# Kernel tuning notes

Measured on AMD Instinct MI355X. Metric: run time of the kernel, lower is better.

Reference implementation:

```python
import jax, jax.numpy as jnp
import numpy as np
import math

B, S, E, DH = 4, 2048, 2048, 256
NEG_INF = jnp.float32(-jnp.inf)


def setup_inputs() -> dict:
    key = jax.random.key(0)
    kx, kq, kk, kv, kp = jax.random.split(key, 5)
    xav = math.sqrt(6.0 / (E + DH))  # xavier_uniform bound
    x = jax.random.normal(kx, (B, S, E), dtype=jnp.float32)
    W_Q = jax.random.uniform(kq, (E, DH), dtype=jnp.float32, minval=-xav, maxval=xav)
    W_K = jax.random.uniform(kk, (E, DH), dtype=jnp.float32, minval=-xav, maxval=xav)
    W_V = jax.random.uniform(kv, (E, DH), dtype=jnp.float32, minval=-xav, maxval=xav)
    b_Q = jnp.zeros((DH,), dtype=jnp.float32)
    b_K = jnp.zeros((DH,), dtype=jnp.float32)
    b_V = jnp.zeros((DH,), dtype=jnp.float32)
    causal_mask = jnp.tril(jnp.ones((S, S), dtype=jnp.int32))  # 1 = attend
    padding_mask = jax.random.randint(kp, (B, S), 0, 2) == 1  # True = masked key
    padding_mask = padding_mask.at[:, 0].set(False)  # keep key 0 valid (avoid all--inf rows)
    return {"x": x, "causal_mask": causal_mask, "padding_mask": padding_mask,
            "W_Q": W_Q, "b_Q": b_Q, "W_K": W_K, "b_K": b_K, "W_V": W_V, "b_V": b_V}


def reference(x, causal_mask, padding_mask, W_Q, b_Q, W_K, b_K, W_V, b_V):
    # Q, K, V projections: [B,S,E] @ [E,DH] -> [B,S,DH]
    Q = x @ W_Q + b_Q
    K = x @ W_K + b_K
    V = x @ W_V + b_V
    scores = jnp.einsum('bqd,bkd->bqk', Q, K) / jnp.sqrt(jnp.float32(DH))
    scores = jnp.where(causal_mask[None, :, :] == 0, NEG_INF, scores)
    scores = jnp.where(padding_mask[:, None, :], NEG_INF, scores)
    attn = jax.nn.softmax(scores, axis=-1)
    return attn @ V  # [B,S,DH]
```

## Files before the change

kernel.cpp:

```cpp
#include <hip/hip_runtime.h>
#include <stdint.h>

typedef float  f32x4  __attribute__((ext_vector_type(4)));
typedef short  s16x8  __attribute__((ext_vector_type(8)));
typedef unsigned int u32x4 __attribute__((ext_vector_type(4)));
typedef unsigned short ushort_t;

#define B_  4
#define S_  2048
#define E_  2048
#define DH_ 256

#define MFMA16(a,b,c) __builtin_amdgcn_mfma_f32_16x16x32_bf16((a),(b),(c),0,0,0)

__device__ __forceinline__ ushort_t f2b(float f){
  unsigned u = __builtin_bit_cast(unsigned, f);
  u += 0x7fffu + ((u >> 16) & 1u);
  return (ushort_t)(u >> 16);
}

__global__ __launch_bounds__(256) void k_convert_x(const float* __restrict__ x,
                                                   ushort_t* __restrict__ xbf){
  size_t i = ((size_t)blockIdx.x * 256 + threadIdx.x) * 8;
  f32x4 a = *(const f32x4*)(x + i);
  f32x4 b = *(const f32x4*)(x + i + 4);
  union { ushort_t us[8]; u32x4 v; } u;
#pragma unroll
  for (int j = 0; j < 4; ++j){ u.us[j] = f2b(a[j]); u.us[4+j] = f2b(b[j]); }
  *(u32x4*)(xbf + i) = u.v;
}

__global__ __launch_bounds__(256) void k_transpose_w(const float* __restrict__ Wq,
                                                     const float* __restrict__ Wk,
                                                     const float* __restrict__ Wv,
                                                     ushort_t* __restrict__ Wt){
  __shared__ ushort_t tile[32][33];
  int z = blockIdx.z;
  const float* W = (z == 0) ? Wq : ((z == 1) ? Wk : Wv);
  int k0 = blockIdx.x * 32, n0 = blockIdx.y * 32;
  int t = threadIdx.x, tx = t & 31, ty = t >> 5;
#pragma unroll
  for (int i = 0; i < 4; ++i)
    tile[ty + i*8][tx] = f2b(W[(size_t)(k0 + ty + i*8) * DH_ + n0 + tx]);
  __syncthreads();
#pragma unroll
  for (int i = 0; i < 4; ++i)
    Wt[(size_t)z * DH_ * E_ + (size_t)(n0 + ty + i*8) * E_ + k0 + tx] = tile[tx][ty + i*8];
}

__global__ __launch_bounds__(256) void k_prep_pad(const unsigned char* __restrict__ pm,
                                                  float* __restrict__ padf){
  const int n = B_ * S_;
  int any = 0;
  for (int i = threadIdx.x; i < n; i += 256)
    if ((i & 3) && pm[i]) any = 1;
  int isb = __syncthreads_or(any);
  for (int i = threadIdx.x; i < n; i += 256){
    unsigned char v = isb ? pm[i] : pm[(size_t)i * 4];
    padf[i] = v ? -__builtin_inff() : 0.0f;
  }
}

__global__ __launch_bounds__(256) void k_gemm_qkv(const ushort_t* __restrict__ xbf,
                                                  const ushort_t* __restrict__ Wt,
                                                  const float* __restrict__ bQ,
                                                  const float* __restrict__ bK,
                                                  const float* __restrict__ bV,
                                                  ushort_t* __restrict__ Qo,
                                                  ushort_t* __restrict__ Ko,
                                                  ushort_t* __restrict__ Vo){
  __shared__ __align__(16) ushort_t Al[64 * 64];
  __shared__ __align__(16) ushort_t Bl[64 * 64];
  int z = blockIdx.z;
  const ushort_t* W = Wt + (size_t)z * DH_ * E_;
  const float* bias = (z == 0) ? bQ : ((z == 1) ? bK : bV);
  ushort_t* out = (z == 0) ? Qo : ((z == 1) ? Ko : Vo);
  int m0 = blockIdx.x * 64, n0 = blockIdx.y * 64;
  int t = threadIdx.x;
  int lane = t & 63, w = t >> 6, lo = lane & 15, grp = lane >> 4;
  f32x4 z4; z4[0] = z4[1] = z4[2] = z4[3] = 0.f;
  f32x4 acc[4] = { z4, z4, z4, z4 };
  int arow = t >> 2;
  int c8a  = t & 3;

  for (int k0 = 0; k0 < E_; k0 += 64){
    __syncthreads();
#pragma unroll
    for (int p = 0; p < 2; ++p){
      int c8 = c8a + p * 4;
      u32x4 av = *(const u32x4*)(xbf + (size_t)(m0 + arow) * E_ + k0 + c8 * 8);
      *(u32x4*)((char*)Al + ((arow * 128 + c8 * 16) ^ ((arow & 7) << 4))) = av;
      u32x4 bv = *(const u32x4*)(W + (size_t)(n0 + arow) * E_ + k0 + c8 * 8);
      *(u32x4*)((char*)Bl + ((arow * 128 + c8 * 16) ^ ((arow & 7) << 4))) = bv;
    }
    __syncthreads();
#pragma unroll
    for (int kk = 0; kk < 2; ++kk){
      int ar = w * 16 + lo;
      s16x8 a = *(const s16x8*)((const char*)Al +
                 ((ar * 128 + kk * 64 + grp * 16) ^ ((ar & 7) << 4)));
#pragma unroll
      for (int nt = 0; nt < 4; ++nt){
        int br = nt * 16 + lo;
        s16x8 b = *(const s16x8*)((const char*)Bl +
                   ((br * 128 + kk * 64 + grp * 16) ^ ((br & 7) << 4)));
        acc[nt] = MFMA16(a, b, acc[nt]);
      }
    }
  }
#pragma unroll
  for (int nt = 0; nt < 4; ++nt){
    int col = n0 + nt * 16 + lo;
    float bb = bias[col];
#pragma unroll
    for (int r = 0; r < 4; ++r){
      int row = m0 + w * 16 + grp * 4 + r;
      out[(size_t)row * DH_ + col] = f2b(acc[nt][r] + bb);
    }
  }
}

__global__ __launch_bounds__(256) void k_transpose_v(const ushort_t* __restrict__ V,
                                                     ushort_t* __restrict__ Vt){
  __shared__ ushort_t tile[32][33];
  int r0 = blockIdx.x * 32, c0 = blockIdx.y * 32;
  int t = threadIdx.x, tx = t & 31, ty = t >> 5;
#pragma unroll
  for (int i = 0; i < 4; ++i)
    tile[ty + i*8][tx] = V[(size_t)(r0 + ty + i*8) * DH_ + c0 + tx];
  __syncthreads();
  int b = r0 >> 11, s0 = r0 & (S_ - 1);
#pragma unroll
  for (int i = 0; i < 4; ++i)
    Vt[(size_t)(b * DH_ + c0 + ty + i*8) * S_ + s0 + tx] = tile[tx][ty + i*8];
}

__global__ __launch_bounds__(512) void k_attn(const ushort_t* __restrict__ Q,
                                              const ushort_t* __restrict__ K,
                                              const ushort_t* __restrict__ Vt,
                                              const float* __restrict__ padf,
                                              float* __restrict__ out){
  __shared__ __align__(16) ushort_t P[8][16][32];
  __shared__ float Osum[16][260];
  __shared__ float ml[8][16][2];
  __shared__ float Linv[16];
  int blk = blockIdx.x;
  int b = blk & (B_ - 1);
  int qt = (S_ / 16 - 1) - (blk >> 2);
  int t = threadIdx.x;
  int lane = t & 63, w = t >> 6, lo = lane & 15, grp = lane >> 4;
  int qbase = qt * 16;
  const float NEG = -__builtin_inff();

  s16x8 aq[8];
#pragma unroll
  for (int d = 0; d < 8; ++d)
    aq[d] = *(const s16x8*)(Q + (size_t)(b * S_ + qbase + lo) * DH_ + d * 32 + grp * 8);

  f32x4 z4; z4[0] = z4[1] = z4[2] = z4[3] = 0.f;
  f32x4 o[16];
#pragma unroll
  for (int i = 0; i < 16; ++i) o[i] = z4;
  float m[4], l[4];
#pragma unroll
  for (int r = 0; r < 4; ++r){ m[r] = NEG; l[r] = 0.f; }

  int qhi = qbase + 15;
  int ntiles = (qhi >> 5) + 1;

  for (int kt = w; kt < ntiles; kt += 8){
    int k0 = kt * 32;
    f32x4 s[2];
#pragma unroll
    for (int h = 0; h < 2; ++h){
      int kb = k0 + h * 16;
      if (kb <= qhi){
        f32x4 acc = z4;
#pragma unroll
        for (int d = 0; d < 8; ++d){
          s16x8 bk = *(const s16x8*)(K + (size_t)(b * S_ + kb + lo) * DH_ + d * 32 + grp * 8);
          acc = MFMA16(aq[d], bk, acc);
        }
        int kcol = kb + lo;
        float pv = padf[b * S_ + kcol];
#pragma unroll
        for (int r = 0; r < 4; ++r){
          int q = qbase + grp * 4 + r;
          float v = acc[r] * 0.0625f + pv;
          s[h][r] = (kcol <= q) ? v : NEG;
        }
      } else {
#pragma unroll
        for (int r = 0; r < 4; ++r) s[h][r] = NEG;
      }
    }
    float alpha[4];
    int need = 0;
#pragma unroll
    for (int r = 0; r < 4; ++r){
      float mr = fmaxf(s[0][r], s[1][r]);
      mr = fmaxf(mr, __shfl_xor(mr, 1));
      mr = fmaxf(mr, __shfl_xor(mr, 2));
      mr = fmaxf(mr, __shfl_xor(mr, 4));
      mr = fmaxf(mr, __shfl_xor(mr, 8));
      float mn = fmaxf(m[r], mr);
      float mexp = (mn == NEG) ? 0.f : mn;
      float al = __expf(m[r] - mexp);
      alpha[r] = al;
      float p0 = __expf(s[0][r] - mexp);
      float p1 = __expf(s[1][r] - mexp);
      s[0][r] = p0; s[1][r] = p1;
      float pr = p0 + p1;
      pr += __shfl_xor(pr, 1);
      pr += __shfl_xor(pr, 2);
      pr += __shfl_xor(pr, 4);
      pr += __shfl_xor(pr, 8);
      l[r] = l[r] * al + pr;
      need |= (mn > m[r]);
      m[r] = mn;
    }
    if (__any(need)){
#pragma unroll
      for (int i = 0; i < 16; ++i)
#pragma unroll
        for (int r = 0; r < 4; ++r) o[i][r] *= alpha[r];
    }
#pragma unroll
    for (int h = 0; h < 2; ++h)
#pragma unroll
      for (int r = 0; r < 4; ++r)
        P[w][grp * 4 + r][h * 16 + lo] = f2b(s[h][r]);
    s16x8 pa = *(const s16x8*)(&P[w][lo][grp * 8]);
#pragma unroll
    for (int i = 0; i < 16; ++i){
      s16x8 vb = *(const s16x8*)(Vt + (size_t)(b * DH_ + i * 16 + lo) * S_ + k0 + grp * 8);
      o[i] = MFMA16(pa, vb, o[i]);
    }
  }

  if (lo == 0){
#pragma unroll
    for (int r = 0; r < 4; ++r){ ml[w][grp * 4 + r][0] = m[r]; ml[w][grp * 4 + r][1] = l[r]; }
  }
  __syncthreads();
  float sc[4];
#pragma unroll
  for (int r = 0; r < 4; ++r){
    int row = grp * 4 + r;
    float Mx = NEG;
#pragma unroll
    for (int ww = 0; ww < 8; ++ww) Mx = fmaxf(Mx, ml[ww][row][0]);
    float Ls = 0.f;
#pragma unroll
    for (int ww = 0; ww < 8; ++ww) Ls += ml[ww][row][1] * __expf(ml[ww][row][0] - Mx);
    sc[r] = __expf(m[r] - Mx);
    if (w == 0 && lo == 0) Linv[row] = 1.0f / Ls;
  }
#pragma unroll
  for (int i = 0; i < 16; ++i)
#pragma unroll
    for (int r = 0; r < 4; ++r) o[i][r] *= sc[r];
  for (int ww = 0; ww < 8; ++ww){
    if (w == ww){
#pragma unroll
      for (int i = 0; i < 16; ++i)
#pragma unroll
        for (int r = 0; r < 4; ++r){
          float* p = &Osum[grp * 4 + r][i * 16 + lo];
          if (ww == 0) *p = o[i][r]; else *p += o[i][r];
        }
    }
    __syncthreads();
  }
  int row = t >> 5, sub = t & 31;
  float li = Linv[row];
  size_t obase = (size_t)(b * S_ + qbase + row) * DH_ + sub * 8;
#pragma unroll
  for (int j = 0; j < 8; ++j)
    out[obase + j] = Osum[row][sub * 8 + j] * li;
}

extern "C" void kernel_launch(void* const* d_in, const int* in_sizes, int n_in,
                              void* d_out, int out_size, void* d_ws, size_t ws_size,
                              hipStream_t stream){
  const float* x          = (const float*)d_in[0];
  const unsigned char* pm = (const unsigned char*)d_in[2];
  const float* Wq = (const float*)d_in[3];
  const float* bQ = (const float*)d_in[4];
  const float* Wk = (const float*)d_in[5];
  const float* bK = (const float*)d_in[6];
  const float* Wv = (const float*)d_in[7];
  const float* bV = (const float*)d_in[8];
  float* out = (float*)d_out;

  char* ws = (char*)d_ws;
  ushort_t* xbf  = (ushort_t*)(ws);
  ushort_t* Wt   = (ushort_t*)(ws + 33554432);
  ushort_t* Qb   = (ushort_t*)(ws + 36700160);
  ushort_t* Kb   = (ushort_t*)(ws + 40894464);
  ushort_t* Vb   = (ushort_t*)(ws + 45088768);
  ushort_t* Vt   = (ushort_t*)(ws + 49283072);
  float*    padf = (float*)  (ws + 53477376);

  k_convert_x  <<<dim3(8192),       dim3(256), 0, stream>>>(x, xbf);
  k_transpose_w<<<dim3(64, 8, 3),   dim3(256), 0, stream>>>(Wq, Wk, Wv, Wt);
  k_prep_pad   <<<dim3(1),          dim3(256), 0, stream>>>(pm, padf);
  k_gemm_qkv   <<<dim3(128, 4, 3),  dim3(256), 0, stream>>>(xbf, Wt, bQ, bK, bV, Qb, Kb, Vb);
  k_transpose_v<<<dim3(256, 8),     dim3(256), 0, stream>>>(Vb, Vt);
  k_attn       <<<dim3(512),        dim3(512), 0, stream>>>(Qb, Kb, Vt, padf, out);
}
```

Before: 300.4 us.

## Enlarge GEMM tile with direct LDS loads and rework attention to 64-key tiles

The QKV GEMM now uses 128x64 tiles with a 2x2 wave layout and loads into LDS with global_load_lds, so the register round trip is dropped and each B tile is reused across more rows. Attention now processes 64-key tiles per wave and computes S transposed, so each lane owns one query row. It adds a lazy max-rescale rule with a threshold of 8 and applies the causal mask only on diagonal tiles. The padding mask is packed into bitmasks instead of a float array. The risks are more register pressure, and possible precision drift from the lazy rescale and the -1e30 sentinel.

```diff
diff --git a/kernel.cpp b/kernel.cpp
--- a/kernel.cpp
+++ b/kernel.cpp
@@ -5,6 +5,7 @@
 typedef short  s16x8  __attribute__((ext_vector_type(8)));
 typedef unsigned int u32x4 __attribute__((ext_vector_type(4)));
 typedef unsigned short ushort_t;
+typedef unsigned int uint_t;
 
 #define B_  4
 #define S_  2048
@@ -12,6 +13,10 @@
 #define DH_ 256
 
 #define MFMA16(a,b,c) __builtin_amdgcn_mfma_f32_16x16x32_bf16((a),(b),(c),0,0,0)
+
+#define GL16(gp, lp) __builtin_amdgcn_global_load_lds( \
+    (const __attribute__((address_space(1))) unsigned int*)(gp), \
+    (__attribute__((address_space(3))) unsigned int*)(lp), 16, 0, 0)
 
 __device__ __forceinline__ ushort_t f2b(float f){
   unsigned u = __builtin_bit_cast(unsigned, f);
@@ -49,16 +54,22 @@
 }
 
 __global__ __launch_bounds__(256) void k_prep_pad(const unsigned char* __restrict__ pm,
-                                                  float* __restrict__ padf){
+                                                  uint_t* __restrict__ padbits){
   const int n = B_ * S_;
   int any = 0;
   for (int i = threadIdx.x; i < n; i += 256)
     if ((i & 3) && pm[i]) any = 1;
   int isb = __syncthreads_or(any);
-  for (int i = threadIdx.x; i < n; i += 256){
-    unsigned char v = isb ? pm[i] : pm[(size_t)i * 4];
-    padf[i] = v ? -__builtin_inff() : 0.0f;
-  }
+  int t = threadIdx.x;
+  uint_t bits = 0;
+  int base = (t >> 6) * S_ + (t & 63) * 32;
+#pragma unroll
+  for (int j = 0; j < 32; ++j){
+    size_t idx = base + j;
+    unsigned char v = isb ? pm[idx] : pm[idx * 4];
+    bits |= (v ? 1u : 0u) << j;
+  }
+  padbits[t] = bits;
 }
 
 __global__ __launch_bounds__(256) void k_gemm_qkv(const ushort_t* __restrict__ xbf,
@@ -69,54 +80,69 @@
                                                   ushort_t* __restrict__ Qo,
                                                   ushort_t* __restrict__ Ko,
                                                   ushort_t* __restrict__ Vo){
-  __shared__ __align__(16) ushort_t Al[64 * 64];
+  __shared__ __align__(16) ushort_t Al[128 * 64];
   __shared__ __align__(16) ushort_t Bl[64 * 64];
   int z = blockIdx.z;
   const ushort_t* W = Wt + (size_t)z * DH_ * E_;
   const float* bias = (z == 0) ? bQ : ((z == 1) ? bK : bV);
   ushort_t* out = (z == 0) ? Qo : ((z == 1) ? Ko : Vo);
-  int m0 = blockIdx.x * 64, n0 = blockIdx.y * 64;
+  int m0 = blockIdx.x * 128, n0 = blockIdx.y * 64;
   int t = threadIdx.x;
   int lane = t & 63, w = t >> 6, lo = lane & 15, grp = lane >> 4;
+  int wm = w >> 1, wn = w & 1;
+  int rA = t >> 3;
+  int jsw = ((t & 7) ^ (rA & 7)) * 8;
+
   f32x4 z4; z4[0] = z4[1] = z4[2] = z4[3] = 0.f;
-  f32x4 acc[4] = { z4, z4, z4, z4 };
-  int arow = t >> 2;
-  int c8a  = t & 3;
+  f32x4 acc[4][2];
+#pragma unroll
+  for (int mt = 0; mt < 4; ++mt){ acc[mt][0] = z4; acc[mt][1] = z4; }
+
+  char* lA = (char*)Al + w * 1024;
+  char* lB = (char*)Bl + w * 1024;
 
   for (int k0 = 0; k0 < E_; k0 += 64){
     __syncthreads();
-#pragma unroll
-    for (int p = 0; p < 2; ++p){
-      int c8 = c8a + p * 4;
-      u32x4 av = *(const u32x4*)(xbf + (size_t)(m0 + arow) * E_ + k0 + c8 * 8);
-      *(u32x4*)((char*)Al + ((arow * 128 + c8 * 16) ^ ((arow & 7) << 4))) = av;
-      u32x4 bv = *(const u32x4*)(W + (size_t)(n0 + arow) * E_ + k0 + c8 * 8);
-      *(u32x4*)((char*)Bl + ((arow * 128 + c8 * 16) ^ ((arow & 7) << 4))) = bv;
-    }
+    const ushort_t* gA = xbf + (size_t)(m0 + rA) * E_ + k0 + jsw;
+    const ushort_t* gB = W   + (size_t)(n0 + rA) * E_ + k0 + jsw;
+#pragma unroll
+    for (int i = 0; i < 4; ++i)
+      GL16(gA + (size_t)i * 32 * E_, lA + i * 4096);
+#pragma unroll
+    for (int i = 0; i < 2; ++i)
+      GL16(gB + (size_t)i * 32 * E_, lB + i * 4096);
     __syncthreads();
 #pragma unroll
     for (int kk = 0; kk < 2; ++kk){
-      int ar = w * 16 + lo;
-      s16x8 a = *(const s16x8*)((const char*)Al +
-                 ((ar * 128 + kk * 64 + grp * 16) ^ ((ar & 7) << 4)));
-#pragma unroll
-      for (int nt = 0; nt < 4; ++nt){
-        int br = nt * 16 + lo;
-        s16x8 b = *(const s16x8*)((const char*)Bl +
-                   ((br * 128 + kk * 64 + grp * 16) ^ ((br & 7) << 4)));
-        acc[nt] = MFMA16(a, b, acc[nt]);
-      }
-    }
-  }
-#pragma unroll
-  for (int nt = 0; nt < 4; ++nt){
-    int col = n0 + nt * 16 + lo;
+      s16x8 av[4], bv[2];
+#pragma unroll
+      for (int mt = 0; mt < 4; ++mt){
+        int row = wm * 64 + mt * 16 + lo;
+        av[mt] = *(const s16x8*)((char*)Al + ((row * 128 + kk * 64 + grp * 16) ^ ((row & 7) << 4)));
+      }
+#pragma unroll
+      for (int nt = 0; nt < 2; ++nt){
+        int row = wn * 32 + nt * 16 + lo;
+        bv[nt] = *(const s16x8*)((char*)Bl + ((row * 128 + kk * 64 + grp * 16) ^ ((row & 7) << 4)));
+      }
+#pragma unroll
+      for (int mt = 0; mt < 4; ++mt)
+#pragma unroll
+        for (int nt = 0; nt < 2; ++nt)
+          acc[mt][nt] = MFMA16(av[mt], bv[nt], acc[mt][nt]);
+    }
+  }
+#pragma unroll
+  for (int nt = 0; nt < 2; ++nt){
+    int col = n0 + wn * 32 + nt * 16 + lo;
     float bb = bias[col];
 #pragma unroll
-    for (int r = 0; r < 4; ++r){
-      int row = m0 + w * 16 + grp * 4 + r;
-      out[(size_t)row * DH_ + col] = f2b(acc[nt][r] + bb);
-    }
+    for (int mt = 0; mt < 4; ++mt)
+#pragma unroll
+      for (int r = 0; r < 4; ++r){
+        int row = m0 + wm * 64 + mt * 16 + grp * 4 + r;
+        out[(size_t)row * DH_ + col] = f2b(acc[mt][nt][r] + bb);
+      }
   }
 }
 
@@ -138,9 +164,9 @@
 __global__ __launch_bounds__(512) void k_attn(const ushort_t* __restrict__ Q,
                                               const ushort_t* __restrict__ K,
                                               const ushort_t* __restrict__ Vt,
-                                              const float* __restrict__ padf,
+                                              const uint_t* __restrict__ padbits,
                                               float* __restrict__ out){
-  __shared__ __align__(16) ushort_t P[8][16][32];
+  __shared__ __align__(16) ushort_t P[8][16][72];
   __shared__ float Osum[16][260];
   __shared__ float ml[8][16][2];
   __shared__ float Linv[16];
@@ -151,6 +177,7 @@
   int lane = t & 63, w = t >> 6, lo = lane & 15, grp = lane >> 4;
   int qbase = qt * 16;
   const float NEG = -__builtin_inff();
+  const float MSENT = -1e30f;
 
   s16x8 aq[8];
 #pragma unroll
@@ -161,105 +188,124 @@
   f32x4 o[16];
 #pragma unroll
   for (int i = 0; i < 16; ++i) o[i] = z4;
-  float m[4], l[4];
-#pragma unroll
-  for (int r = 0; r < 4; ++r){ m[r] = NEG; l[r] = 0.f; }
+  float m_lo = MSENT, l_lo = 0.f;
 
   int qhi = qbase + 15;
-  int ntiles = (qhi >> 5) + 1;
-
-  for (int kt = w; kt < ntiles; kt += 8){
-    int k0 = kt * 32;
-    f32x4 s[2];
-#pragma unroll
-    for (int h = 0; h < 2; ++h){
-      int kb = k0 + h * 16;
-      if (kb <= qhi){
-        f32x4 acc = z4;
-#pragma unroll
-        for (int d = 0; d < 8; ++d){
-          s16x8 bk = *(const s16x8*)(K + (size_t)(b * S_ + kb + lo) * DH_ + d * 32 + grp * 8);
-          acc = MFMA16(aq[d], bk, acc);
-        }
-        int kcol = kb + lo;
-        float pv = padf[b * S_ + kcol];
-#pragma unroll
-        for (int r = 0; r < 4; ++r){
-          int q = qbase + grp * 4 + r;
-          float v = acc[r] * 0.0625f + pv;
-          s[h][r] = (kcol <= q) ? v : NEG;
-        }
-      } else {
-#pragma unroll
-        for (int r = 0; r < 4; ++r) s[h][r] = NEG;
-      }
-    }
-    float alpha[4];
-    int need = 0;
-#pragma unroll
-    for (int r = 0; r < 4; ++r){
-      float mr = fmaxf(s[0][r], s[1][r]);
-      mr = fmaxf(mr, __shfl_xor(mr, 1));
-      mr = fmaxf(mr, __shfl_xor(mr, 2));
-      mr = fmaxf(mr, __shfl_xor(mr, 4));
-      mr = fmaxf(mr, __shfl_xor(mr, 8));
-      float mn = fmaxf(m[r], mr);
-      float mexp = (mn == NEG) ? 0.f : mn;
-      float al = __expf(m[r] - mexp);
-      alpha[r] = al;
-      float p0 = __expf(s[0][r] - mexp);
-      float p1 = __expf(s[1][r] - mexp);
-      s[0][r] = p0; s[1][r] = p1;
-      float pr = p0 + p1;
-      pr += __shfl_xor(pr, 1);
-      pr += __shfl_xor(pr, 2);
-      pr += __shfl_xor(pr, 4);
-      pr += __shfl_xor(pr, 8);
-      l[r] = l[r] * al + pr;
-      need |= (mn > m[r]);
-      m[r] = mn;
-    }
-    if (__any(need)){
-#pragma unroll
-      for (int i = 0; i < 16; ++i)
-#pragma unroll
-        for (int r = 0; r < 4; ++r) o[i][r] *= alpha[r];
-    }
-#pragma unroll
-    for (int h = 0; h < 2; ++h)
-#pragma unroll
-      for (int r = 0; r < 4; ++r)
-        P[w][grp * 4 + r][h * 16 + lo] = f2b(s[h][r]);
-    s16x8 pa = *(const s16x8*)(&P[w][lo][grp * 8]);
+  int nt64 = (qhi >> 6) + 1;
+
+  for (int kt = w; kt < nt64; kt += 8){
+    int k0 = kt * 64;
+    bool full = (k0 + 63 <= qbase);
+    f32x4 sc[4];
+#pragma unroll
+    for (int h = 0; h < 4; ++h) sc[h] = z4;
+#pragma unroll
+    for (int d = 0; d < 8; ++d){
+#pragma unroll
+      for (int h = 0; h < 4; ++h){
+        s16x8 kf = *(const s16x8*)(K + (size_t)(b * S_ + k0 + h * 16 + lo) * DH_ + d * 32 + grp * 8);
+        sc[h] = MFMA16(kf, aq[d], sc[h]);
+      }
+    }
+    uint_t pb0 = padbits[b * 64 + kt * 2];
+    uint_t pb1 = padbits[b * 64 + kt * 2 + 1];
+#pragma unroll
+    for (int h = 0; h < 4; ++h){
+      uint_t bg = ((h < 2 ? pb0 : pb1) >> ((h & 1) * 16)) >> (4 * grp);
+#pragma unroll
+      for (int r = 0; r < 4; ++r){
+        float v = sc[h][r] * 0.0625f;
+        sc[h][r] = ((bg >> r) & 1) ? NEG : v;
+      }
+    }
+    if (!full){
+#pragma unroll
+      for (int h = 0; h < 4; ++h)
+#pragma unroll
+        for (int r = 0; r < 4; ++r)
+          if (k0 + h * 16 + 4 * grp + r > qbase + lo) sc[h][r] = NEG;
+    }
+    float mt0 = fmaxf(fmaxf(sc[0][0], sc[0][1]), fmaxf(sc[0][2], sc[0][3]));
+    float mt1 = fmaxf(fmaxf(sc[1][0], sc[1][1]), fmaxf(sc[1][2], sc[1][3]));
+    float mt2 = fmaxf(fmaxf(sc[2][0], sc[2][1]), fmaxf(sc[2][2], sc[2][3]));
+    float mt3 = fmaxf(fmaxf(sc[3][0], sc[3][1]), fmaxf(sc[3][2], sc[3][3]));
+    float mt = fmaxf(fmaxf(mt0, mt1), fmaxf(mt2, mt3));
+    mt = fmaxf(mt, __shfl_xor(mt, 16));
+    mt = fmaxf(mt, __shfl_xor(mt, 32));
+    if (__any(mt > m_lo + 8.f)){
+      float mn = fmaxf(m_lo, mt);
+      float al = __expf(m_lo - mn);
+      m_lo = mn;
+      l_lo *= al;
+      float a0 = __shfl(al, 4 * grp + 0);
+      float a1 = __shfl(al, 4 * grp + 1);
+      float a2 = __shfl(al, 4 * grp + 2);
+      float a3 = __shfl(al, 4 * grp + 3);
+#pragma unroll
+      for (int i = 0; i < 16; ++i){
+        o[i][0] *= a0; o[i][1] *= a1; o[i][2] *= a2; o[i][3] *= a3;
+      }
+    }
+    float ls = 0.f;
+#pragma unroll
+    for (int h = 0; h < 4; ++h)
+#pragma unroll
+      for (int r = 0; r < 4; ++r){
+        float p = __expf(sc[h][r] - m_lo);
+        sc[h][r] = p;
+        ls += p;
+      }
+    ls += __shfl_xor(ls, 16);
+    ls += __shfl_xor(ls, 32);
+    l_lo += ls;
+    char* prow = (char*)&P[w][lo][0];
+#pragma unroll
+    for (int h = 0; h < 4; ++h){
+      uint_t u0 = (uint_t)f2b(sc[h][0]) | ((uint_t)f2b(sc[h][1]) << 16);
+      uint_t u1 = (uint_t)f2b(sc[h][2]) | ((uint_t)f2b(sc[h][3]) << 16);
+      *(uint_t*)(prow + h * 32 + grp * 8)     = u0;
+      *(uint_t*)(prow + h * 32 + grp * 8 + 4) = u1;
+    }
+    s16x8 pa0 = *(const s16x8*)(prow + grp * 16);
+    s16x8 pa1 = *(const s16x8*)(prow + 64 + grp * 16);
 #pragma unroll
     for (int i = 0; i < 16; ++i){
-      s16x8 vb = *(const s16x8*)(Vt + (size_t)(b * DH_ + i * 16 + lo) * S_ + k0 + grp * 8);
-      o[i] = MFMA16(pa, vb, o[i]);
-    }
+      s16x8 v0 = *(const s16x8*)(Vt + (size_t)(b * DH_ + i * 16 + lo) * S_ + k0 + grp * 8);
+      s16x8 v1 = *(const s16x8*)(Vt + (size_t)(b * DH_ + i * 16 + lo) * S_ + k0 + 32 + grp * 8);
+      o[i] = MFMA16(pa0, v0, o[i]);
+      o[i] = MFMA16(pa1, v1, o[i]);
+    }
+  }
+
+  float mo[4], lo_[4];
+#pragma unroll
+  for (int r = 0; r < 4; ++r){
+    mo[r]  = __shfl(m_lo, 4 * grp + r);
+    lo_[r] = __shfl(l_lo, 4 * grp + r);
   }
 
   if (lo == 0){
 #pragma unroll
-    for (int r = 0; r < 4; ++r){ ml[w][grp * 4 + r][0] = m[r]; ml[w][grp * 4 + r][1] = l[r]; }
+    for (int r = 0; r < 4; ++r){ ml[w][grp * 4 + r][0] = mo[r]; ml[w][grp * 4 + r][1] = lo_[r]; }
   }
   __syncthreads();
-  float sc[4];
+  float sc2[4];
 #pragma unroll
   for (int r = 0; r < 4; ++r){
     int row = grp * 4 + r;
-    float Mx = NEG;
+    float Mx = MSENT;
 #pragma unroll
     for (int ww = 0; ww < 8; ++ww) Mx = fmaxf(Mx, ml[ww][row][0]);
     float Ls = 0.f;
 #pragma unroll
     for (int ww = 0; ww < 8; ++ww) Ls += ml[ww][row][1] * __expf(ml[ww][row][0] - Mx);
-    sc[r] = __expf(m[r] - Mx);
+    sc2[r] = __expf(mo[r] - Mx);
     if (w == 0 && lo == 0) Linv[row] = 1.0f / Ls;
   }
 #pragma unroll
   for (int i = 0; i < 16; ++i)
 #pragma unroll
-    for (int r = 0; r < 4; ++r) o[i][r] *= sc[r];
+    for (int r = 0; r < 4; ++r) o[i][r] *= sc2[r];
   for (int ww = 0; ww < 8; ++ww){
     if (w == ww){
 #pragma unroll
@@ -300,12 +346,12 @@
   ushort_t* Kb   = (ushort_t*)(ws + 40894464);
   ushort_t* Vb   = (ushort_t*)(ws + 45088768);
   ushort_t* Vt   = (ushort_t*)(ws + 49283072);
-  float*    padf = (float*)  (ws + 53477376);
+  uint_t*   padbits = (uint_t*)(ws + 53477376);
 
   k_convert_x  <<<dim3(8192),       dim3(256), 0, stream>>>(x, xbf);
   k_transpose_w<<<dim3(64, 8, 3),   dim3(256), 0, stream>>>(Wq, Wk, Wv, Wt);
-  k_prep_pad   <<<dim3(1),          dim3(256), 0, stream>>>(pm, padf);
-  k_gemm_qkv   <<<dim3(128, 4, 3),  dim3(256), 0, stream>>>(xbf, Wt, bQ, bK, bV, Qb, Kb, Vb);
+  k_prep_pad   <<<dim3(1),          dim3(256), 0, stream>>>(pm, padbits);
+  k_gemm_qkv   <<<dim3(64, 4, 3),   dim3(256), 0, stream>>>(xbf, Wt, bQ, bK, bV, Qb, Kb, Vb);
   k_transpose_v<<<dim3(256, 8),     dim3(256), 0, stream>>>(Vb, Vt);
-  k_attn       <<<dim3(512),        dim3(512), 0, stream>>>(Qb, Kb, Vt, padf, out);
-}
+  k_attn       <<<dim3(512),        dim3(512), 0, stream>>>(Qb, Kb, Vt, padbits, out);
+}
```

Result: faster. 266.8 us (-11.2%).
